# Performance work log

Measured on AMD Instinct MI355X. Metric: run time of the kernel, lower is better.

Reference implementation:

```python
import jax, jax.numpy as jnp
import numpy as np

EPS = 1e-20


def squash(s):
    # n: [..., 1] norm over last axis
    n = jnp.linalg.norm(s, axis=-1, keepdims=True)
    return (1.0 - 1.0 / (jnp.exp(n) + EPS)) * (s / (n + EPS))


def setup_inputs() -> dict:
    key = jax.random.key(0)
    k1, k2 = jax.random.split(key)
    B, iN, iD, N, D = 1024, 128, 16, 32, 32
    inputs = jax.random.normal(k1, (B, iN, iD), dtype=jnp.float32)
    # he_normal: std = sqrt(2 / fan_in), fan_in = iN*iD (per keras conventions on 4D weight)
    fan_in = iN * iD
    W = jax.random.normal(k2, (N, iN, iD, D), dtype=jnp.float32) * np.sqrt(2.0 / fan_in).astype(np.float32)
    b = jnp.zeros((N, iN, 1), dtype=jnp.float32)
    return {"inputs": inputs, "W": W, "b": b}


def reference(inputs, W, b):
    D = W.shape[-1]
    # u[b,n,j,z] = sum_i inputs[b,j,i] * W[n,j,i,z]  -> [B, N, iN, D]
    u = jnp.einsum('bji,njiz->bnjz', inputs, W)
    # c[b,n,i] = sum_k sum_j u[b,n,i,j] * u[b,n,k,j] = u[b,n,i,:] . sum_k u[b,n,k,:]
    usum = jnp.sum(u, axis=2)                      # [B, N, D]
    c = jnp.einsum('bnid,bnd->bni', u, usum)[..., None]  # [B, N, iN, 1]
    c = c / jnp.sqrt(jnp.float32(D))
    c = jax.nn.softmax(c, axis=1)                  # softmax over parent-capsule axis N
    c = c + b                                      # b broadcasts over batch
    s = jnp.sum(u * c, axis=-2)                    # [B, N, D]
    return squash(s)
```

## Files before the change

kernel.cpp:

```cpp
#include <hip/hip_runtime.h>
#include <math.h>

#define B_TOT 1024
#define IN_N  128
#define IN_D  16
#define NCAP  32
#define DCAP  32

typedef __attribute__((ext_vector_type(8)))  short bf16x8;
typedef __attribute__((ext_vector_type(16))) float f32x16;
typedef unsigned int  uint_;
typedef unsigned short ushort_;

__device__ __forceinline__ uint_ cvt_pk_bf16(float lo, float hi) {
    uint_ r;
    asm("v_cvt_pk_bf16_f32 %0, %1, %2" : "=v"(r) : "v"(lo), "v"(hi));
    return r;
}
__device__ __forceinline__ float bf16_to_f(ushort_ h) {
    return __uint_as_float(((uint_)h) << 16);
}

__global__ __launch_bounds__(256)
void prep(const float* __restrict__ x, const float* __restrict__ W,
          ushort_* __restrict__ XW, ushort_* __restrict__ WT) {
    const int blk = blockIdx.x;
    const int t   = threadIdx.x;

    if (blk < 512) {
        const int q  = blk * 256 + t;
        const int z  = q & 31;
        const int nj = q >> 5;
        const float* p = W + (size_t)nj * (IN_D * DCAP) + z;
        float f[16];
#pragma unroll
        for (int i = 0; i < 16; ++i) f[i] = p[i * 32];
        uint4 lo, hi;
        lo.x = cvt_pk_bf16(f[0],  f[1]);  lo.y = cvt_pk_bf16(f[2],  f[3]);
        lo.z = cvt_pk_bf16(f[4],  f[5]);  lo.w = cvt_pk_bf16(f[6],  f[7]);
        hi.x = cvt_pk_bf16(f[8],  f[9]);  hi.y = cvt_pk_bf16(f[10], f[11]);
        hi.z = cvt_pk_bf16(f[12], f[13]); hi.w = cvt_pk_bf16(f[14], f[15]);
        uint4* dst = (uint4*)(WT + (size_t)q * 16);
        dst[0] = lo; dst[1] = hi;
        return;
    }

    const int id = blk - 512;
    const int tb = id >> 5;
    const int tc = id & 31;
    const int b0 = tb * 64, c0 = tc * 64;

    __shared__ uint2 lds8[64][16];

    {
        const int c4 = t & 15;
#pragma unroll
        for (int k = 0; k < 4; ++k) {
            const int r = (t >> 4) + 16 * k;
            const float4 f = *(const float4*)(x + (size_t)(b0 + r) * 2048 + c0 + c4 * 4);
            uint2 o;
            o.x = cvt_pk_bf16(f.x, f.y);
            o.y = cvt_pk_bf16(f.z, f.w);
            lds8[r][c4 ^ (r & 15)] = o;
        }
    }
    __syncthreads();

    const int jb2l = t >> 5;
    const int jb20 = tc * 8;
#pragma unroll
    for (int h = 0; h < 2; ++h) {
        const int bl = (t & 31) + h * 32;
        const uint2 u0 = lds8[bl][(jb2l * 2)     ^ (bl & 15)];
        const uint2 u1 = lds8[bl][(jb2l * 2 + 1) ^ (bl & 15)];
        uint4 o; o.x = u0.x; o.y = u0.y; o.z = u1.x; o.w = u1.y;
        *(uint4*)(XW + ((size_t)(jb20 + jb2l) * 1024 + b0 + bl) * 8) = o;
    }
}

__global__ __launch_bounds__(256, 4)
void kA(const ushort_* __restrict__ XW, const ushort_* __restrict__ WT,
        ushort_* __restrict__ LC) {
    const int bid = blockIdx.x;
    const int n   = bid >> 5;
    const int cb0 = (bid & 31) * 32;
    const int t   = threadIdx.x;
    const int wv  = t >> 6;
    const int l   = t & 63;
    const int lo5 = l & 31;
    const int hi  = l >> 5;

    __shared__ float xch[4][16 * 64];

    const ushort_* aBase = WT + ((size_t)(n * IN_N) * 32 + lo5) * 16 + (size_t)hi * 8;
    const ushort_* bBase = XW + ((size_t)hi * 1024 + cb0 + lo5) * 8;

    const int jbeg = wv * 32;

    f32x16 us0, us1, us2, us3;
#pragma unroll
    for (int r = 0; r < 16; ++r) { us0[r] = 0.f; us1[r] = 0.f; us2[r] = 0.f; us3[r] = 0.f; }

    for (int j = jbeg; j < jbeg + 32; j += 4) {
        bf16x8 a0 = *(const bf16x8*)(aBase + (size_t)j * 512);
        bf16x8 x0 = *(const bf16x8*)(bBase + (size_t)j * 16384);
        bf16x8 a1 = *(const bf16x8*)(aBase + (size_t)(j + 1) * 512);
        bf16x8 x1 = *(const bf16x8*)(bBase + (size_t)(j + 1) * 16384);
        us0 = __builtin_amdgcn_mfma_f32_32x32x16_bf16(a0, x0, us0, 0, 0, 0);
        us1 = __builtin_amdgcn_mfma_f32_32x32x16_bf16(a1, x1, us1, 0, 0, 0);
        bf16x8 a2 = *(const bf16x8*)(aBase + (size_t)(j + 2) * 512);
        bf16x8 x2 = *(const bf16x8*)(bBase + (size_t)(j + 2) * 16384);
        bf16x8 a3 = *(const bf16x8*)(aBase + (size_t)(j + 3) * 512);
        bf16x8 x3 = *(const bf16x8*)(bBase + (size_t)(j + 3) * 16384);
        us2 = __builtin_amdgcn_mfma_f32_32x32x16_bf16(a2, x2, us2, 0, 0, 0);
        us3 = __builtin_amdgcn_mfma_f32_32x32x16_bf16(a3, x3, us3, 0, 0, 0);
    }
#pragma unroll
    for (int r = 0; r < 16; ++r)
        us0[r] = (us0[r] + us1[r]) + (us2[r] + us3[r]);

#pragma unroll
    for (int r = 0; r < 16; ++r) xch[wv][r * 64 + l] = us0[r];
    __syncthreads();

    f32x16 us;
#pragma unroll
    for (int r = 0; r < 16; ++r)
        us[r] = (xch[0][r * 64 + l] + xch[1][r * 64 + l]) +
                (xch[2][r * 64 + l] + xch[3][r * 64 + l]);

    const float rsqD = 0.17677669529663689f;
    f32x16 zc;
#pragma unroll
    for (int r = 0; r < 16; ++r) zc[r] = 0.f;

    for (int jb = jbeg + 28; jb >= jbeg; jb -= 4) {
        bf16x8 a0 = *(const bf16x8*)(aBase + (size_t)jb * 512);
        bf16x8 x0 = *(const bf16x8*)(bBase + (size_t)jb * 16384);
        bf16x8 a1 = *(const bf16x8*)(aBase + (size_t)(jb + 1) * 512);
        bf16x8 x1 = *(const bf16x8*)(bBase + (size_t)(jb + 1) * 16384);
        bf16x8 a2 = *(const bf16x8*)(aBase + (size_t)(jb + 2) * 512);
        bf16x8 x2 = *(const bf16x8*)(bBase + (size_t)(jb + 2) * 16384);
        bf16x8 a3 = *(const bf16x8*)(aBase + (size_t)(jb + 3) * 512);
        bf16x8 x3 = *(const bf16x8*)(bBase + (size_t)(jb + 3) * 16384);
        f32x16 u0 = __builtin_amdgcn_mfma_f32_32x32x16_bf16(a0, x0, zc, 0, 0, 0);
        f32x16 u1 = __builtin_amdgcn_mfma_f32_32x32x16_bf16(a1, x1, zc, 0, 0, 0);
        f32x16 u2 = __builtin_amdgcn_mfma_f32_32x32x16_bf16(a2, x2, zc, 0, 0, 0);
        f32x16 u3 = __builtin_amdgcn_mfma_f32_32x32x16_bf16(a3, x3, zc, 0, 0, 0);

        float p0a = u0[0] * us[0], p0b = u0[1] * us[1];
        float p1a = u1[0] * us[0], p1b = u1[1] * us[1];
        float p2a = u2[0] * us[0], p2b = u2[1] * us[1];
        float p3a = u3[0] * us[0], p3b = u3[1] * us[1];
#pragma unroll
        for (int r = 2; r < 16; r += 2) {
            p0a = fmaf(u0[r], us[r], p0a); p0b = fmaf(u0[r + 1], us[r + 1], p0b);
            p1a = fmaf(u1[r], us[r], p1a); p1b = fmaf(u1[r + 1], us[r + 1], p1b);
            p2a = fmaf(u2[r], us[r], p2a); p2b = fmaf(u2[r + 1], us[r + 1], p2b);
            p3a = fmaf(u3[r], us[r], p3a); p3b = fmaf(u3[r + 1], us[r + 1], p3b);
        }
        float p0 = p0a + p0b, p1 = p1a + p1b, p2 = p2a + p2b, p3 = p3a + p3b;
        p0 += __shfl_xor(p0, 32);
        p1 += __shfl_xor(p1, 32);
        p2 += __shfl_xor(p2, 32);
        p3 += __shfl_xor(p3, 32);
        const float q01 = (hi ? p1 : p0) * rsqD;
        const float q23 = (hi ? p3 : p2) * rsqD;
        uint_ k01 = cvt_pk_bf16(q01, q01);
        uint_ k23 = cvt_pk_bf16(q23, q23);
        LC[(size_t)(n * IN_N + jb + hi) * 1024 + cb0 + lo5]     = (ushort_)(k01 & 0xffffu);
        LC[(size_t)(n * IN_N + jb + 2 + hi) * 1024 + cb0 + lo5] = (ushort_)(k23 & 0xffffu);
    }
}

__global__ __launch_bounds__(256)
void kB(const float* __restrict__ bias, ushort_* __restrict__ LC) {
    const int t = blockIdx.x * 256 + threadIdx.x;
    const int j = t >> 10;
    const int b = t & 1023;
    float v[NCAP];
    float m = -1e30f;
#pragma unroll
    for (int n = 0; n < NCAP; ++n) {
        v[n] = bf16_to_f(LC[(size_t)(n * IN_N + j) * 1024 + b]);
        m = fmaxf(m, v[n]);
    }
    float s = 0.f;
#pragma unroll
    for (int n = 0; n < NCAP; ++n) { v[n] = __expf(v[n] - m); s += v[n]; }
    const float inv = 1.f / s;
#pragma unroll
    for (int n = 0; n < NCAP; ++n) {
        const float c = v[n] * inv + bias[n * IN_N + j];
        uint_ pk = cvt_pk_bf16(c, c);
        LC[(size_t)(n * IN_N + j) * 1024 + b] = (ushort_)(pk & 0xffffu);
    }
}

__global__ __launch_bounds__(256, 4)
void kC(const ushort_* __restrict__ XW, const ushort_* __restrict__ WT,
        const ushort_* __restrict__ LC, float* __restrict__ out) {
    const int bid = blockIdx.x;
    const int n   = bid >> 5;
    const int cb0 = (bid & 31) * 32;
    const int t   = threadIdx.x;
    const int wv  = t >> 6;
    const int l   = t & 63;
    const int lo5 = l & 31;
    const int hi  = l >> 5;

    __shared__ float xch[3][16 * 64];

    const ushort_* aBase = WT + ((size_t)(n * IN_N) * 32 + lo5) * 16 + (size_t)hi * 8;
    const ushort_* bBase = XW + ((size_t)hi * 1024 + cb0 + lo5) * 8;
    const ushort_* cBase = LC + (size_t)(n * IN_N) * 1024 + cb0 + lo5;

    f32x16 s0, zc;
#pragma unroll
    for (int r = 0; r < 16; ++r) { s0[r] = 0.f; zc[r] = 0.f; }

    const int jbeg = wv * 32;
    for (int jb = jbeg; jb < jbeg + 32; jb += 4) {
        bf16x8 a0 = *(const bf16x8*)(aBase + (size_t)jb * 512);
        bf16x8 x0 = *(const bf16x8*)(bBase + (size_t)jb * 16384);
        bf16x8 a1 = *(const bf16x8*)(aBase + (size_t)(jb + 1) * 512);
        bf16x8 x1 = *(const bf16x8*)(bBase + (size_t)(jb + 1) * 16384);
        bf16x8 a2 = *(const bf16x8*)(aBase + (size_t)(jb + 2) * 512);
        bf16x8 x2 = *(const bf16x8*)(bBase + (size_t)(jb + 2) * 16384);
        bf16x8 a3 = *(const bf16x8*)(aBase + (size_t)(jb + 3) * 512);
        bf16x8 x3 = *(const bf16x8*)(bBase + (size_t)(jb + 3) * 16384);
        const float c0 = bf16_to_f(cBase[(size_t)jb * 1024]);
        const float c1 = bf16_to_f(cBase[(size_t)(jb + 1) * 1024]);
        const float c2 = bf16_to_f(cBase[(size_t)(jb + 2) * 1024]);
        const float c3 = bf16_to_f(cBase[(size_t)(jb + 3) * 1024]);
        f32x16 u0 = __builtin_amdgcn_mfma_f32_32x32x16_bf16(a0, x0, zc, 0, 0, 0);
        f32x16 u1 = __builtin_amdgcn_mfma_f32_32x32x16_bf16(a1, x1, zc, 0, 0, 0);
        f32x16 u2 = __builtin_amdgcn_mfma_f32_32x32x16_bf16(a2, x2, zc, 0, 0, 0);
        f32x16 u3 = __builtin_amdgcn_mfma_f32_32x32x16_bf16(a3, x3, zc, 0, 0, 0);
#pragma unroll
        for (int r = 0; r < 16; ++r) {
            float acc = fmaf(c0, u0[r], s0[r]);
            acc = fmaf(c1, u1[r], acc);
            acc = fmaf(c2, u2[r], acc);
            s0[r] = fmaf(c3, u3[r], acc);
        }
    }

    if (wv > 0) {
#pragma unroll
        for (int r = 0; r < 16; ++r) xch[wv - 1][r * 64 + l] = s0[r];
    }
    __syncthreads();

    if (wv == 0) {
#pragma unroll
        for (int r = 0; r < 16; ++r)
            s0[r] += (xch[0][r * 64 + l] + xch[1][r * 64 + l]) + xch[2][r * 64 + l];
        float q0 = s0[0] * s0[0], q1 = s0[1] * s0[1];
        float q2 = s0[2] * s0[2], q3 = s0[3] * s0[3];
#pragma unroll
        for (int r = 4; r < 16; r += 4) {
            q0 = fmaf(s0[r],     s0[r],     q0);
            q1 = fmaf(s0[r + 1], s0[r + 1], q1);
            q2 = fmaf(s0[r + 2], s0[r + 2], q2);
            q3 = fmaf(s0[r + 3], s0[r + 3], q3);
        }
        float q = (q0 + q1) + (q2 + q3);
        q += __shfl_xor(q, 32);
        const float nn = sqrtf(q);
        const float f  = (1.f - 1.f / (__expf(nn) + 1e-20f)) / (nn + 1e-20f);
        float* op = out + ((size_t)(cb0 + lo5) * NCAP + n) * DCAP + hi * 4;
#pragma unroll
        for (int g = 0; g < 4; ++g) {
            float4 v4 = { s0[g*4] * f, s0[g*4+1] * f, s0[g*4+2] * f, s0[g*4+3] * f };
            *(float4*)(op + g * 8) = v4;
        }
    }
}

extern "C" void kernel_launch(void* const* d_in, const int* in_sizes, int n_in,
                              void* d_out, int out_size, void* d_ws, size_t ws_size,
                              hipStream_t stream) {
    const float* x    = (const float*)d_in[0];
    const float* W    = (const float*)d_in[1];
    const float* bias = (const float*)d_in[2];
    float* out = (float*)d_out;

    char* ws = (char*)d_ws;
    ushort_* XW = (ushort_*)ws;
    ushort_* WT = (ushort_*)(ws + (4u << 20));
    ushort_* LC = (ushort_*)(ws + (8u << 20));

    prep<<<1024, 256, 0, stream>>>(x, W, XW, WT);
    kA<<<1024, 256, 0, stream>>>(XW, WT, LC);
    kB<<<512, 256, 0, stream>>>(bias, LC);
    kC<<<1024, 256, 0, stream>>>(XW, WT, LC, out);
}
```

Before: 54.02 us.

## Merge kA/kC into 1024-thread blocks covering two capsules and 64 batches

```diff
diff --git a/kernel.cpp b/kernel.cpp
--- a/kernel.cpp
+++ b/kernel.cpp
@@ -78,24 +78,31 @@
     }
 }
 
-__global__ __launch_bounds__(256, 4)
+__global__ __launch_bounds__(1024, 4)
 void kA(const ushort_* __restrict__ XW, const ushort_* __restrict__ WT,
         ushort_* __restrict__ LC) {
-    const int bid = blockIdx.x;
-    const int n   = bid >> 5;
-    const int cb0 = (bid & 31) * 32;
+    const int raw = blockIdx.x;
+    const int bid = ((raw & 7) << 5) | (raw >> 3);
+    const int np  = bid >> 4;
+    const int bt  = bid & 15;
     const int t   = threadIdx.x;
-    const int wv  = t >> 6;
+    const int w   = t >> 6;
     const int l   = t & 63;
     const int lo5 = l & 31;
     const int hi  = l >> 5;
-
-    __shared__ float xch[4][16 * 64];
+    const int nsub = w >> 3;
+    const int bh   = (w >> 2) & 1;
+    const int jw   = w & 3;
+
+    const int n   = np * 2 + nsub;
+    const int cb0 = bt * 64 + bh * 32;
+
+    __shared__ float xch[16][1024];
 
     const ushort_* aBase = WT + ((size_t)(n * IN_N) * 32 + lo5) * 16 + (size_t)hi * 8;
     const ushort_* bBase = XW + ((size_t)hi * 1024 + cb0 + lo5) * 8;
 
-    const int jbeg = wv * 32;
+    const int jbeg = jw * 32;
 
     f32x16 us0, us1, us2, us3;
 #pragma unroll
@@ -119,15 +126,26 @@
     for (int r = 0; r < 16; ++r)
         us0[r] = (us0[r] + us1[r]) + (us2[r] + us3[r]);
 
-#pragma unroll
-    for (int r = 0; r < 16; ++r) xch[wv][r * 64 + l] = us0[r];
+    {
+        float4* d = (float4*)&xch[w][l * 16];
+#pragma unroll
+        for (int g = 0; g < 4; ++g)
+            d[g] = (float4){us0[g*4], us0[g*4+1], us0[g*4+2], us0[g*4+3]};
+    }
     __syncthreads();
 
+    const int wg = w & ~3;
     f32x16 us;
 #pragma unroll
-    for (int r = 0; r < 16; ++r)
-        us[r] = (xch[0][r * 64 + l] + xch[1][r * 64 + l]) +
-                (xch[2][r * 64 + l] + xch[3][r * 64 + l]);
+    for (int g = 0; g < 4; ++g) {
+        float4 s = (float4){0.f, 0.f, 0.f, 0.f};
+#pragma unroll
+        for (int ww = 0; ww < 4; ++ww) {
+            const float4 a = *(const float4*)&xch[wg + ww][l * 16 + g * 4];
+            s.x += a.x; s.y += a.y; s.z += a.z; s.w += a.w;
+        }
+        us[g*4] = s.x; us[g*4+1] = s.y; us[g*4+2] = s.z; us[g*4+3] = s.w;
+    }
 
     const float rsqD = 0.17677669529663689f;
     f32x16 zc;
@@ -197,19 +215,26 @@
     }
 }
 
-__global__ __launch_bounds__(256, 4)
+__global__ __launch_bounds__(1024, 4)
 void kC(const ushort_* __restrict__ XW, const ushort_* __restrict__ WT,
         const ushort_* __restrict__ LC, float* __restrict__ out) {
-    const int bid = blockIdx.x;
-    const int n   = bid >> 5;
-    const int cb0 = (bid & 31) * 32;
+    const int raw = blockIdx.x;
+    const int bid = ((raw & 7) << 5) | (raw >> 3);
+    const int np  = bid >> 4;
+    const int bt  = bid & 15;
     const int t   = threadIdx.x;
-    const int wv  = t >> 6;
+    const int w   = t >> 6;
     const int l   = t & 63;
     const int lo5 = l & 31;
     const int hi  = l >> 5;
-
-    __shared__ float xch[3][16 * 64];
+    const int nsub = w >> 3;
+    const int bh   = (w >> 2) & 1;
+    const int jw   = w & 3;
+
+    const int n   = np * 2 + nsub;
+    const int cb0 = bt * 64 + bh * 32;
+
+    __shared__ float xch[16][1024];
 
     const ushort_* aBase = WT + ((size_t)(n * IN_N) * 32 + lo5) * 16 + (size_t)hi * 8;
     const ushort_* bBase = XW + ((size_t)hi * 1024 + cb0 + lo5) * 8;
@@ -219,7 +244,7 @@
 #pragma unroll
     for (int r = 0; r < 16; ++r) { s0[r] = 0.f; zc[r] = 0.f; }
 
-    const int jbeg = wv * 32;
+    const int jbeg = jw * 32;
     for (int jb = jbeg; jb < jbeg + 32; jb += 4) {
         bf16x8 a0 = *(const bf16x8*)(aBase + (size_t)jb * 512);
         bf16x8 x0 = *(const bf16x8*)(bBase + (size_t)jb * 16384);
@@ -246,16 +271,25 @@
         }
     }
 
-    if (wv > 0) {
-#pragma unroll
-        for (int r = 0; r < 16; ++r) xch[wv - 1][r * 64 + l] = s0[r];
+    if (jw > 0) {
+        float4* d = (float4*)&xch[w][l * 16];
+#pragma unroll
+        for (int g = 0; g < 4; ++g)
+            d[g] = (float4){s0[g*4], s0[g*4+1], s0[g*4+2], s0[g*4+3]};
     }
     __syncthreads();
 
-    if (wv == 0) {
-#pragma unroll
-        for (int r = 0; r < 16; ++r)
-            s0[r] += (xch[0][r * 64 + l] + xch[1][r * 64 + l]) + xch[2][r * 64 + l];
+    if (jw == 0) {
+        const int wg = w;
+#pragma unroll
+        for (int g = 0; g < 4; ++g) {
+#pragma unroll
+            for (int ww = 1; ww < 4; ++ww) {
+                const float4 a = *(const float4*)&xch[wg + ww][l * 16 + g * 4];
+                s0[g*4]   += a.x; s0[g*4+1] += a.y;
+                s0[g*4+2] += a.z; s0[g*4+3] += a.w;
+            }
+        }
         float q0 = s0[0] * s0[0], q1 = s0[1] * s0[1];
         float q2 = s0[2] * s0[2], q3 = s0[3] * s0[3];
 #pragma unroll
@@ -292,7 +326,7 @@
     ushort_* LC = (ushort_*)(ws + (8u << 20));
 
     prep<<<1024, 256, 0, stream>>>(x, W, XW, WT);
-    kA<<<1024, 256, 0, stream>>>(XW, WT, LC);
+    kA<<<256, 1024, 0, stream>>>(XW, WT, LC);
     kB<<<512, 256, 0, stream>>>(bias, LC);
-    kC<<<1024, 256, 0, stream>>>(XW, WT, LC, out);
-}
+    kC<<<256, 1024, 0, stream>>>(XW, WT, LC, out);
+}
```

Measured after the change: 54.80 us. About the same (+1.4%).
